# Optimization experiments

Measured on AMD Instinct MI355X. Metric: run time of the kernel, lower is better.

Reference implementation:

```python
import jax, jax.numpy as jnp
import numpy as np

LN_EPS = 1e-6

def _ln_proj(x, ln_scale, ln_bias, kernel, bias):
    # LayerNorm over last dim, then GEMM projection. Dropout is identity
    # (deterministic / eval mode, training=False default).
    mu = jnp.mean(x, axis=-1, keepdims=True)
    var = jnp.mean(jnp.square(x - mu), axis=-1, keepdims=True)
    xn = (x - mu) * jax.lax.rsqrt(var + LN_EPS) * ln_scale + ln_bias
    return jnp.einsum('bsh,hp->bsp', xn, kernel) + bias


def setup_inputs() -> dict:
    key = jax.random.key(0)
    ks = jax.random.split(key, 4)
    B, S, H, P = 2, 4096, 4096, 1024
    return {
        'vision_features': jax.random.normal(ks[0], (B, S, H), dtype=jnp.float32),
        'text_features': jax.random.normal(ks[1], (B, S, H), dtype=jnp.float32),
        'v_ln_scale': jnp.ones((H,), jnp.float32),
        'v_ln_bias': jnp.zeros((H,), jnp.float32),
        'v_kernel': jax.random.normal(ks[2], (H, P), dtype=jnp.float32) / np.sqrt(H).astype(np.float32),
        'v_bias': jnp.zeros((P,), jnp.float32),
        't_ln_scale': jnp.ones((H,), jnp.float32),
        't_ln_bias': jnp.zeros((H,), jnp.float32),
        't_kernel': jax.random.normal(ks[3], (H, P), dtype=jnp.float32) / np.sqrt(H).astype(np.float32),
        't_bias': jnp.zeros((P,), jnp.float32),
    }


def reference(vision_features, text_features, v_ln_scale, v_ln_bias, v_kernel, v_bias,
              t_ln_scale, t_ln_bias, t_kernel, t_bias):
    vision_projected = _ln_proj(vision_features, v_ln_scale, v_ln_bias, v_kernel, v_bias)
    text_projected = _ln_proj(text_features, t_ln_scale, t_ln_bias, t_kernel, t_bias)
    return (vision_projected, text_projected)
```

## Files before the change

### kernel.cpp

```cpp
#include <hip/hip_runtime.h>
#include <hip/hip_bf16.h>
#include <stdint.h>

#define LN_EPS 1e-6f

typedef __bf16 bf16x8 __attribute__((ext_vector_type(8)));
typedef float f32x4 __attribute__((ext_vector_type(4)));

__device__ __forceinline__ unsigned short f2bf(float f) {
    uint32_t u = __float_as_uint(f);
    uint32_t r = (u + 0x7fffu + ((u >> 16) & 1u)) >> 16;
    return (unsigned short)r;
}

__device__ __forceinline__ void async_copy16(const void* g, void* l) {
    const __attribute__((address_space(1))) uint32_t* gp =
        (const __attribute__((address_space(1))) uint32_t*)(uintptr_t)g;
    __attribute__((address_space(3))) uint32_t* lp =
        (__attribute__((address_space(3))) uint32_t*)(uint32_t)(uintptr_t)l;
    __builtin_amdgcn_global_load_lds(gp, lp, 16, 0, 0);
}

__global__ __launch_bounds__(256) void ln_bf16_kernel(
    const float* __restrict__ x0, const float* __restrict__ x1,
    const float* __restrict__ s0, const float* __restrict__ b0,
    const float* __restrict__ s1, const float* __restrict__ b1,
    unsigned short* __restrict__ y0, unsigned short* __restrict__ y1, int H)
{
    int wave = threadIdx.x >> 6, lane = threadIdx.x & 63;
    int row = blockIdx.x * 4 + wave;
    int prob = blockIdx.y;
    const float* x = (prob ? x1 : x0) + (size_t)row * H;
    const float* s = prob ? s1 : s0;
    const float* b = prob ? b1 : b0;
    unsigned short* y = (prob ? y1 : y0) + (size_t)row * H;

    float4 v[16];
    float sum = 0.f, sq = 0.f;
#pragma unroll
    for (int g = 0; g < 16; ++g) {
        v[g] = ((const float4*)x)[lane + 64 * g];
        sum += v[g].x + v[g].y + v[g].z + v[g].w;
        sq  += v[g].x * v[g].x + v[g].y * v[g].y + v[g].z * v[g].z + v[g].w * v[g].w;
    }
#pragma unroll
    for (int off = 32; off > 0; off >>= 1) {
        sum += __shfl_xor(sum, off, 64);
        sq  += __shfl_xor(sq, off, 64);
    }
    float mu = sum * (1.0f / 4096.0f);
    float var = sq * (1.0f / 4096.0f) - mu * mu;
    float rstd = rsqrtf(var + LN_EPS);

#pragma unroll
    for (int g = 0; g < 16; ++g) {
        int i4 = lane + 64 * g;
        float4 sc = ((const float4*)s)[i4];
        float4 bi = ((const float4*)b)[i4];
        ushort4 o;
        o.x = f2bf((v[g].x - mu) * rstd * sc.x + bi.x);
        o.y = f2bf((v[g].y - mu) * rstd * sc.y + bi.y);
        o.z = f2bf((v[g].z - mu) * rstd * sc.z + bi.z);
        o.w = f2bf((v[g].w - mu) * rstd * sc.w + bi.w);
        ((ushort4*)y)[i4] = o;
    }
}

__global__ __launch_bounds__(256) void cast_transpose_kernel(
    const float* __restrict__ w0, const float* __restrict__ w1,
    unsigned short* __restrict__ o0, unsigned short* __restrict__ o1,
    int K, int N)
{
    int prob = blockIdx.z;
    const float* w = prob ? w1 : w0;
    unsigned short* o = prob ? o1 : o0;
    __shared__ unsigned short tile[32][33];
    int tx = threadIdx.x & 31;
    int ty = threadIdx.x >> 5;
    int n0 = blockIdx.x * 32;
    int k0 = blockIdx.y * 32;
#pragma unroll
    for (int i = 0; i < 4; ++i) {
        int k = ty + 8 * i;
        tile[k][tx] = f2bf(w[(size_t)(k0 + k) * N + n0 + tx]);
    }
    __syncthreads();
#pragma unroll
    for (int i = 0; i < 4; ++i) {
        int n = ty + 8 * i;
        o[(size_t)(n0 + n) * K + k0 + tx] = tile[tx][n];
    }
}

#define BM 128
#define BN 128
#define BK 64

__global__ __launch_bounds__(256) void gemm_bf16_kernel(
    const unsigned short* __restrict__ A0, const unsigned short* __restrict__ A1,
    const unsigned short* __restrict__ W0, const unsigned short* __restrict__ W1,
    const float* __restrict__ bias0, const float* __restrict__ bias1,
    float* __restrict__ out0, float* __restrict__ out1,
    int M, int N, int K)
{
    int id = blockIdx.x;
    int xcd = id & 7;
    int l = id >> 3;
    int prob = l >> 6;
    int rem = l & 63;
    int mt = xcd * 8 + (rem >> 3);
    int nt = rem & 7;

    const unsigned short* A = prob ? A1 : A0;
    const unsigned short* W = prob ? W1 : W0;
    const float* bias = prob ? bias1 : bias0;
    float* out = prob ? out1 : out0;

    __shared__ unsigned short As[2 * BM * BK];
    __shared__ unsigned short Bs[2 * BM * BK];

    int t = threadIdx.x;
    int wave = t >> 6, lane = t & 63;
    int quad = lane >> 4, r16 = lane & 15;
    int wm = wave >> 1, wn = wave & 1;
    int kx = r16 & 7;

    int tile_m = mt * BM;
    int tile_n = nt * BN;

    const unsigned short* ga[4];
    const unsigned short* gb[4];
    uint32_t lb[4];
#pragma unroll
    for (int q = 0; q < 4; ++q) {
        int cc = q * 256 + t;
        int row = cc >> 3, kb = cc & 7;
        int kbg = kb ^ (row & 7);
        ga[q] = A + (size_t)(tile_m + row) * K + kbg * 8;
        gb[q] = W + (size_t)(tile_n + row) * K + kbg * 8;
        lb[q] = (uint32_t)(q * 256 + wave * 64) * 16;
    }

    f32x4 acc[4][4] = {};

#pragma unroll
    for (int q = 0; q < 4; ++q) {
        async_copy16(ga[q], (char*)As + lb[q]);
        async_copy16(gb[q], (char*)Bs + lb[q]);
    }
    __syncthreads();

    const int NTILES = K >> 6;
    for (int kt = 0; kt < NTILES; ++kt) {
        const int cur = kt & 1;
        const unsigned short* cA = As + cur * (BM * BK);
        const unsigned short* cB = Bs + cur * (BM * BK);

        if (kt + 1 < NTILES) {
            const int ko = (kt + 1) << 6;
            char* dA = (char*)As + (cur ^ 1) * (BM * BK * 2);
            char* dB = (char*)Bs + (cur ^ 1) * (BM * BK * 2);
#pragma unroll
            for (int q = 0; q < 4; ++q) {
                async_copy16(ga[q] + ko, dA + lb[q]);
                async_copy16(gb[q] + ko, dB + lb[q]);
            }
        }

#pragma unroll
        for (int s = 0; s < 2; ++s) {
            bf16x8 af[4], bfr[4];
#pragma unroll
            for (int i = 0; i < 4; ++i) {
                int ka = (s * 4 + quad) ^ kx;
                af[i]  = *(const bf16x8*)(cA + (wm * 64 + i * 16 + r16) * 64 + ka * 8);
                bfr[i] = *(const bf16x8*)(cB + (wn * 64 + i * 16 + r16) * 64 + ka * 8);
            }
#pragma unroll
            for (int i = 0; i < 4; ++i)
#pragma unroll
                for (int j = 0; j < 4; ++j)
                    acc[i][j] = __builtin_amdgcn_mfma_f32_16x16x32_bf16(af[i], bfr[j], acc[i][j], 0, 0, 0);
        }

        __syncthreads();
    }

#pragma unroll
    for (int j = 0; j < 4; ++j) {
        int col = tile_n + wn * 64 + j * 16 + r16;
        float bj = bias[col];
#pragma unroll
        for (int i = 0; i < 4; ++i) {
            int row = tile_m + wm * 64 + i * 16 + quad * 4;
#pragma unroll
            for (int r = 0; r < 4; ++r)
                out[(size_t)(row + r) * N + col] = acc[i][j][r] + bj;
        }
    }
}

extern "C" void kernel_launch(void* const* d_in, const int* in_sizes, int n_in,
                              void* d_out, int out_size, void* d_ws, size_t ws_size,
                              hipStream_t stream) {
    const float* xv = (const float*)d_in[0];
    const float* xt = (const float*)d_in[1];
    const float* sv = (const float*)d_in[2];
    const float* bv = (const float*)d_in[3];
    const float* wv = (const float*)d_in[4];
    const float* biasv = (const float*)d_in[5];
    const float* st = (const float*)d_in[6];
    const float* bt = (const float*)d_in[7];
    const float* wt = (const float*)d_in[8];
    const float* biast = (const float*)d_in[9];
    float* out = (float*)d_out;

    const int B = 2, S = 4096, H = 4096, P = 1024;
    const int M = B * S;
    float* outv = out;
    float* outt = out + (size_t)M * P;

    size_t xnBytes = (size_t)M * H * 2;
    size_t wtBytes = (size_t)P * H * 2;
    char* ws = (char*)d_ws;

    if (ws_size >= 2 * xnBytes + 2 * wtBytes) {
        unsigned short* Xv = (unsigned short*)(ws);
        unsigned short* Xt = (unsigned short*)(ws + xnBytes);
        unsigned short* Wv = (unsigned short*)(ws + 2 * xnBytes);
        unsigned short* Wt = (unsigned short*)(ws + 2 * xnBytes + wtBytes);
        ln_bf16_kernel<<<dim3(M / 4, 2), 256, 0, stream>>>(xv, xt, sv, bv, st, bt, Xv, Xt, H);
        cast_transpose_kernel<<<dim3(P / 32, H / 32, 2), 256, 0, stream>>>(wv, wt, Wv, Wt, H, P);
        gemm_bf16_kernel<<<dim3(1024), 256, 0, stream>>>(
            Xv, Xt, Wv, Wt, biasv, biast, outv, outt, M, P, H);
    } else {
        unsigned short* X  = (unsigned short*)(ws);
        unsigned short* Wb = (unsigned short*)(ws + xnBytes);
        ln_bf16_kernel<<<dim3(M / 4, 1), 256, 0, stream>>>(xv, xv, sv, bv, sv, bv, X, X, H);
        cast_transpose_kernel<<<dim3(P / 32, H / 32, 1), 256, 0, stream>>>(wv, wv, Wb, Wb, H, P);
        gemm_bf16_kernel<<<dim3(512), 256, 0, stream>>>(
            X, X, Wb, Wb, biasv, biasv, outv, outv, M, P, H);
        ln_bf16_kernel<<<dim3(M / 4, 1), 256, 0, stream>>>(xt, xt, st, bt, st, bt, X, X, H);
        cast_transpose_kernel<<<dim3(P / 32, H / 32, 1), 256, 0, stream>>>(wt, wt, Wb, Wb, H, P);
        gemm_bf16_kernel<<<dim3(512), 256, 0, stream>>>(
            X, X, Wb, Wb, biast, biast, outt, outt, M, P, H);
    }
}
```

Measured before the change: 499.0 us.

## Enlarge GEMM M-tile to 256 with BK 32 and 8x4 accumulators per wave

Changes the GEMM block tile from 128x128x64 to 256x128x32, so each wave computes a 128x64 sub-tile with 8x4 MFMA accumulators and reuses each loaded B fragment across 8 A fragments. The shared-memory swizzle and load mapping are reworked for the 32-wide K slab, and the grid is halved to 512 blocks with launch_bounds asking for 2 blocks per CU. The aim is higher arithmetic intensity per LDS and global byte. In exchange there are twice as many K iterations and barriers, more accumulator registers, and only 512 blocks to fill the GPU.

```diff
diff --git a/kernel.cpp b/kernel.cpp
--- a/kernel.cpp
+++ b/kernel.cpp
@@ -92,11 +92,11 @@
     }
 }
 
-#define BM 128
+#define BM 256
 #define BN 128
-#define BK 64
-
-__global__ __launch_bounds__(256) void gemm_bf16_kernel(
+#define BK 32
+
+__global__ __launch_bounds__(256, 2) void gemm_bf16_kernel(
     const unsigned short* __restrict__ A0, const unsigned short* __restrict__ A1,
     const unsigned short* __restrict__ W0, const unsigned short* __restrict__ W1,
     const float* __restrict__ bias0, const float* __restrict__ bias1,
@@ -106,9 +106,9 @@
     int id = blockIdx.x;
     int xcd = id & 7;
     int l = id >> 3;
-    int prob = l >> 6;
-    int rem = l & 63;
-    int mt = xcd * 8 + (rem >> 3);
+    int prob = l >> 5;
+    int rem = l & 31;
+    int mt = xcd * 4 + (rem >> 3);
     int nt = rem & 7;
 
     const unsigned short* A = prob ? A1 : A0;
@@ -117,70 +117,76 @@
     float* out = prob ? out1 : out0;
 
     __shared__ unsigned short As[2 * BM * BK];
-    __shared__ unsigned short Bs[2 * BM * BK];
+    __shared__ unsigned short Bs[2 * BN * BK];
 
     int t = threadIdx.x;
     int wave = t >> 6, lane = t & 63;
     int quad = lane >> 4, r16 = lane & 15;
     int wm = wave >> 1, wn = wave & 1;
-    int kx = r16 & 7;
+    int kx = r16 & 3;
 
     int tile_m = mt * BM;
     int tile_n = nt * BN;
 
     const unsigned short* ga[4];
-    const unsigned short* gb[4];
-    uint32_t lb[4];
+    const unsigned short* gb[2];
+    uint32_t lba[4], lbb[2];
 #pragma unroll
     for (int q = 0; q < 4; ++q) {
         int cc = q * 256 + t;
-        int row = cc >> 3, kb = cc & 7;
-        int kbg = kb ^ (row & 7);
+        int row = cc >> 2, kb = cc & 3;
+        int kbg = kb ^ (row & 3);
         ga[q] = A + (size_t)(tile_m + row) * K + kbg * 8;
+        lba[q] = (uint32_t)(q * 256 + wave * 64) * 16;
+    }
+#pragma unroll
+    for (int q = 0; q < 2; ++q) {
+        int cc = q * 256 + t;
+        int row = cc >> 2, kb = cc & 3;
+        int kbg = kb ^ (row & 3);
         gb[q] = W + (size_t)(tile_n + row) * K + kbg * 8;
-        lb[q] = (uint32_t)(q * 256 + wave * 64) * 16;
-    }
-
-    f32x4 acc[4][4] = {};
-
-#pragma unroll
-    for (int q = 0; q < 4; ++q) {
-        async_copy16(ga[q], (char*)As + lb[q]);
-        async_copy16(gb[q], (char*)Bs + lb[q]);
-    }
+        lbb[q] = (uint32_t)(q * 256 + wave * 64) * 16;
+    }
+
+    f32x4 acc[8][4] = {};
+
+#pragma unroll
+    for (int q = 0; q < 4; ++q) async_copy16(ga[q], (char*)As + lba[q]);
+#pragma unroll
+    for (int q = 0; q < 2; ++q) async_copy16(gb[q], (char*)Bs + lbb[q]);
     __syncthreads();
 
-    const int NTILES = K >> 6;
+    const int NTILES = K >> 5;
     for (int kt = 0; kt < NTILES; ++kt) {
         const int cur = kt & 1;
         const unsigned short* cA = As + cur * (BM * BK);
-        const unsigned short* cB = Bs + cur * (BM * BK);
+        const unsigned short* cB = Bs + cur * (BN * BK);
 
         if (kt + 1 < NTILES) {
-            const int ko = (kt + 1) << 6;
+            const int ko = (kt + 1) << 5;
             char* dA = (char*)As + (cur ^ 1) * (BM * BK * 2);
-            char* dB = (char*)Bs + (cur ^ 1) * (BM * BK * 2);
-#pragma unroll
-            for (int q = 0; q < 4; ++q) {
-                async_copy16(ga[q] + ko, dA + lb[q]);
-                async_copy16(gb[q] + ko, dB + lb[q]);
-            }
-        }
-
-#pragma unroll
-        for (int s = 0; s < 2; ++s) {
-            bf16x8 af[4], bfr[4];
-#pragma unroll
-            for (int i = 0; i < 4; ++i) {
-                int ka = (s * 4 + quad) ^ kx;
-                af[i]  = *(const bf16x8*)(cA + (wm * 64 + i * 16 + r16) * 64 + ka * 8);
-                bfr[i] = *(const bf16x8*)(cB + (wn * 64 + i * 16 + r16) * 64 + ka * 8);
-            }
-#pragma unroll
-            for (int i = 0; i < 4; ++i)
-#pragma unroll
-                for (int j = 0; j < 4; ++j)
-                    acc[i][j] = __builtin_amdgcn_mfma_f32_16x16x32_bf16(af[i], bfr[j], acc[i][j], 0, 0, 0);
+            char* dB = (char*)Bs + (cur ^ 1) * (BN * BK * 2);
+#pragma unroll
+            for (int q = 0; q < 4; ++q) async_copy16(ga[q] + ko, dA + lba[q]);
+#pragma unroll
+            for (int q = 0; q < 2; ++q) async_copy16(gb[q] + ko, dB + lbb[q]);
+        }
+
+        bf16x8 bfr[4];
+#pragma unroll
+        for (int j = 0; j < 4; ++j) {
+            int row = wn * 64 + j * 16 + r16;
+            int ka = quad ^ kx;
+            bfr[j] = *(const bf16x8*)(cB + row * 32 + ka * 8);
+        }
+#pragma unroll
+        for (int i = 0; i < 8; ++i) {
+            int row = wm * 128 + i * 16 + r16;
+            int ka = quad ^ kx;
+            bf16x8 af = *(const bf16x8*)(cA + row * 32 + ka * 8);
+#pragma unroll
+            for (int j = 0; j < 4; ++j)
+                acc[i][j] = __builtin_amdgcn_mfma_f32_16x16x32_bf16(af, bfr[j], acc[i][j], 0, 0, 0);
         }
 
         __syncthreads();
@@ -191,8 +197,8 @@
         int col = tile_n + wn * 64 + j * 16 + r16;
         float bj = bias[col];
 #pragma unroll
-        for (int i = 0; i < 4; ++i) {
-            int row = tile_m + wm * 64 + i * 16 + quad * 4;
+        for (int i = 0; i < 8; ++i) {
+            int row = tile_m + wm * 128 + i * 16 + quad * 4;
 #pragma unroll
             for (int r = 0; r < 4; ++r)
                 out[(size_t)(row + r) * N + col] = acc[i][j][r] + bj;
@@ -231,18 +237,18 @@
         unsigned short* Wt = (unsigned short*)(ws + 2 * xnBytes + wtBytes);
         ln_bf16_kernel<<<dim3(M / 4, 2), 256, 0, stream>>>(xv, xt, sv, bv, st, bt, Xv, Xt, H);
         cast_transpose_kernel<<<dim3(P / 32, H / 32, 2), 256, 0, stream>>>(wv, wt, Wv, Wt, H, P);
-        gemm_bf16_kernel<<<dim3(1024), 256, 0, stream>>>(
+        gemm_bf16_kernel<<<dim3(512), 256, 0, stream>>>(
             Xv, Xt, Wv, Wt, biasv, biast, outv, outt, M, P, H);
     } else {
         unsigned short* X  = (unsigned short*)(ws);
         unsigned short* Wb = (unsigned short*)(ws + xnBytes);
         ln_bf16_kernel<<<dim3(M / 4, 1), 256, 0, stream>>>(xv, xv, sv, bv, sv, bv, X, X, H);
         cast_transpose_kernel<<<dim3(P / 32, H / 32, 1), 256, 0, stream>>>(wv, wv, Wb, Wb, H, P);
-        gemm_bf16_kernel<<<dim3(512), 256, 0, stream>>>(
+        gemm_bf16_kernel<<<dim3(256), 256, 0, stream>>>(
             X, X, Wb, Wb, biasv, biasv, outv, outv, M, P, H);
         ln_bf16_kernel<<<dim3(M / 4, 1), 256, 0, stream>>>(xt, xt, st, bt, st, bt, X, X, H);
         cast_transpose_kernel<<<dim3(P / 32, H / 32, 1), 256, 0, stream>>>(wt, wt, Wb, Wb, H, P);
-        gemm_bf16_kernel<<<dim3(512), 256, 0, stream>>>(
+        gemm_bf16_kernel<<<dim3(256), 256, 0, stream>>>(
             X, X, Wb, Wb, biast, biast, outt, outt, M, P, H);
     }
 }
```

New measurement: 481.6 us. 3.5% less time.
